# Kernel optimization log

Measured on AMD Instinct MI355X. Metric: run time of the kernel, lower is better.

## Reference

```python
import jax, jax.numpy as jnp
import numpy as np

ALPHA = 0.0005
BETA = 0.1
MARGIN = 100.0
GCN_WEIGHT = 0.1
EPS = 1e-8


def _bce(pred, tgt):
    # torch.nn.BCELoss with mean reduction (pred already in (0,1))
    return -jnp.mean(tgt * jnp.log(pred) + (1.0 - tgt) * jnp.log(1.0 - pred))


def _gcn_loss(nodes, labels, sample_idx):
    # nodes: [B, M, D], labels: [B, M] in {-1,0,1}, sample_idx: [B, S]
    n2 = jnp.sum(nodes * nodes, axis=-1)                               # [B, M]
    s_nodes = jnp.take_along_axis(nodes, sample_idx[:, :, None], axis=1)  # [B, S, D]
    s_lab = jnp.take_along_axis(labels, sample_idx, axis=1)            # [B, S]
    s2 = jnp.take_along_axis(n2, sample_idx, axis=1)                   # [B, S]
    cross = jnp.einsum('bsd,bmd->bsm', s_nodes, nodes)                 # [B, S, M]
    d2 = jnp.maximum(s2[:, :, None] + n2[:, None, :] - 2.0 * cross, 0.0)
    valid = labels >= 0
    same = (labels[:, None, :] == s_lab[:, :, None]) & valid[:, None, :]
    opp = (labels[:, None, :] != s_lab[:, :, None]) & valid[:, None, :]
    BIG = jnp.float32(1e30)
    # farthest same-label node, closest opposite-label node (L2 distance; sqrt is monotone)
    pos_idx = jnp.argmax(jnp.where(same, d2, -BIG), axis=-1)           # [B, S]
    neg_idx = jnp.argmin(jnp.where(opp, d2, BIG), axis=-1)             # [B, S]
    s_norm = jnp.sqrt(s2)

    def _cos(idx):
        dot = jnp.take_along_axis(cross, idx[:, :, None], axis=2)[..., 0]
        nb = jnp.sqrt(jnp.take_along_axis(n2, idx, axis=1))
        return dot / (jnp.maximum(s_norm, EPS) * jnp.maximum(nb, EPS))

    pos_loss = jnp.where(jnp.any(same, axis=-1), _cos(pos_idx), 0.0)
    neg_loss = jnp.where(jnp.any(opp, axis=-1), _cos(neg_idx), 0.0)
    return jnp.sum(pos_loss + neg_loss)


def setup_inputs() -> dict:
    key = jax.random.key(0)
    ks = jax.random.split(key, 10)
    B, T, D, C, M, S = 32, 750, 2048, 20, 750, 64
    score_act = jax.random.uniform(ks[0], (B, C)) * 0.98 + 0.01   # sigmoid-like probs in (0,1)
    score_bkg = jax.random.uniform(ks[1], (B, C)) * 0.98 + 0.01
    feat_act = jax.random.normal(ks[2], (B, T, D))
    feat_bkg = jax.random.normal(ks[3], (B, T, D))
    label = (jax.random.uniform(ks[4], (B, C)) < 0.3).astype(jnp.float32)
    label = label.at[:, 0].set(1.0)  # guarantee >=1 positive class per video
    gt = jax.random.uniform(ks[5], (B, T, C))
    cas = jax.random.normal(ks[6], (B, T, C))
    nodes = jax.random.normal(ks[7], (B, M, D))
    nodes_label = jax.random.randint(ks[8], (B, M), 0, 2)
    sample_idx = jax.random.randint(ks[9], (B, S), 0, M)
    return {'score_act': score_act, 'score_bkg': score_bkg, 'feat_act': feat_act,
            'feat_bkg': feat_bkg, 'label': label, 'gt': gt, 'cas': cas,
            'nodes': nodes, 'nodes_label': nodes_label, 'sample_idx': sample_idx}


def reference(score_act, score_bkg, feat_act, feat_bkg, label, gt, cas, nodes, nodes_label, sample_idx):
    label_n = label / jnp.sum(label, axis=1, keepdims=True)
    loss_cls = _bce(score_act, label_n)
    label_bkg = jnp.ones_like(label) / label.shape[1]
    loss_be = _bce(score_bkg, label_bkg)
    loss_act = jnp.maximum(MARGIN - jnp.linalg.norm(jnp.mean(feat_act, axis=1), axis=1), 0.0)
    loss_bkg = jnp.linalg.norm(jnp.mean(feat_bkg, axis=1), axis=1)
    loss_um = jnp.mean((loss_act + loss_bkg) ** 2)
    loss_gcn = GCN_WEIGHT * _gcn_loss(nodes, nodes_label, sample_idx)
    return loss_cls + ALPHA * loss_um + BETA * loss_be + loss_gcn
```

## Files before the change

kernel.cpp:

```cpp
#include <hip/hip_runtime.h>
#include <math.h>

#define BB 32
#define TT 750
#define DD 2048
#define CC 20
#define MM 750
#define SS 64
#define MT 64
#define NT 12
#define FSPLIT 16
#define FROWS 47
#define FUNITS (2 * BB * FSPLIT)

#define ALPHA_W 0.0005f
#define BETA_W 0.1f
#define MARGIN_W 100.0f
#define GCN_W 0.1f
#define EPS_V 1e-8f

#define WS_LOSS01 0
#define WS_N2ACT 16
#define WS_N2BKG 48
#define WS_GCNB 80
#define WS_S2 128
#define WS_CAND 4096
#define WS_COLSUM 200704

typedef __attribute__((ext_vector_type(8))) short bf16x8;
typedef __attribute__((ext_vector_type(4))) float f32x4;

__device__ __forceinline__ unsigned short f2bf(float f) {
  unsigned int u = __float_as_uint(f);
  return (unsigned short)((u + 0x7FFFu + ((u >> 16) & 1u)) >> 16);
}

__global__ __launch_bounds__(512) void feat_kernel(
    const float* __restrict__ feat_act, const float* __restrict__ feat_bkg,
    float* __restrict__ ws) {
  int u = blockIdx.x;
  int tid = threadIdx.x;
  int tz = u >> 9;
  int rem = u & 511;
  int fb = rem >> 4;
  int sub = rem & 15;
  const float* feat = tz ? feat_bkg : feat_act;
  int t0 = sub * FROWS;
  int t1 = t0 + FROWS < TT ? t0 + FROWS : TT;
  const float* bp = feat + (size_t)fb * TT * DD + tid * 4;

  f32x4 a0 = {0.f, 0.f, 0.f, 0.f}, a1 = {0.f, 0.f, 0.f, 0.f};
  f32x4 a2 = {0.f, 0.f, 0.f, 0.f}, a3 = {0.f, 0.f, 0.f, 0.f};
  int t = t0;
  for (; t + 3 < t1; t += 4) {
    f32x4 v0 = __builtin_nontemporal_load((const f32x4*)(bp + (size_t)t * DD));
    f32x4 v1 =
        __builtin_nontemporal_load((const f32x4*)(bp + (size_t)(t + 1) * DD));
    f32x4 v2 =
        __builtin_nontemporal_load((const f32x4*)(bp + (size_t)(t + 2) * DD));
    f32x4 v3 =
        __builtin_nontemporal_load((const f32x4*)(bp + (size_t)(t + 3) * DD));
    a0 += v0;
    a1 += v1;
    a2 += v2;
    a3 += v3;
  }
  for (; t < t1; ++t)
    a0 += __builtin_nontemporal_load((const f32x4*)(bp + (size_t)t * DD));
  f32x4 r = (a0 + a2) + (a1 + a3);
  float* cs =
      ws + WS_COLSUM + ((size_t)(tz * BB + fb) * FSPLIT + sub) * DD + tid * 4;
  *(f32x4*)cs = r;
}

__global__ __launch_bounds__(256, 3) void gcn_kernel(
    const float* __restrict__ score_act, const float* __restrict__ score_bkg,
    const float* __restrict__ label, const float* __restrict__ nodes,
    const int* __restrict__ nlab, const int* __restrict__ sidx,
    float* __restrict__ ws) {
  int bx = blockIdx.x;
  int tid = threadIdx.x;

  if (bx < NT * BB) {
    int b = bx / NT, tile = bx % NT;

    __shared__ __align__(16) unsigned short sAh[64 * 64];
    __shared__ __align__(16) unsigned short sBh[64 * 64];
    __shared__ float sS2[SS];
    __shared__ float sN2[MT];
    __shared__ int sSlab[SS];
    __shared__ int sMlab[MT];

    if (tid < SS) {
      sSlab[tid] = nlab[b * MM + sidx[b * SS + tid]];
    } else if (tid < SS + MT) {
      int ml = tid - SS;
      int m = tile * MT + ml;
      sMlab[ml] = (m < MM) ? nlab[b * MM + m] : -2;
    }

    int r = tid >> 2, p = tid & 3;
    const float* aRow = nodes + ((size_t)b * MM + sidx[b * SS + r]) * DD;
    int mrow = tile * MT + r;
    bool bval = (mrow < MM);
    const float* bRow = nodes + ((size_t)b * MM + (bval ? mrow : 0)) * DD;

    int wslot[4];
#pragma unroll
    for (int j = 0; j < 4; ++j) {
      int u = p + 4 * j;
      wslot[j] = r * 64 + ((((u >> 1) ^ (r & 7)) << 1) + (u & 1)) * 4;
    }

    int lane = tid & 63, w = tid >> 6;
    int g = lane >> 4, c = lane & 15;

    float aSq = 0.f, bSq = 0.f;
    f32x4 acc[4];
#pragma unroll
    for (int f = 0; f < 4; ++f) acc[f] = (f32x4){0.f, 0.f, 0.f, 0.f};

    float4 pa[4], pb[4];
#pragma unroll
    for (int j = 0; j < 4; ++j) {
      int off = (p + 4 * j) * 4;
      pa[j] = *(const float4*)(aRow + off);
      pb[j] = *(const float4*)(bRow + off);
    }

    for (int ch = 0; ch < 32; ++ch) {
      __syncthreads();
#pragma unroll
      for (int j = 0; j < 4; ++j) {
        float4 v = pa[j];
        aSq += v.x * v.x + v.y * v.y + v.z * v.z + v.w * v.w;
        unsigned int lo = (unsigned int)f2bf(v.x) | ((unsigned int)f2bf(v.y) << 16);
        unsigned int hi = (unsigned int)f2bf(v.z) | ((unsigned int)f2bf(v.w) << 16);
        *(uint2*)&sAh[wslot[j]] = make_uint2(lo, hi);
        float4 t = pb[j];
        bSq += t.x * t.x + t.y * t.y + t.z * t.z + t.w * t.w;
        lo = (unsigned int)f2bf(t.x) | ((unsigned int)f2bf(t.y) << 16);
        hi = (unsigned int)f2bf(t.z) | ((unsigned int)f2bf(t.w) << 16);
        *(uint2*)&sBh[wslot[j]] = make_uint2(lo, hi);
      }
      __syncthreads();
      if (ch < 31) {
        const float* ap = aRow + (ch + 1) * 64;
        const float* bp = bRow + (ch + 1) * 64;
#pragma unroll
        for (int j = 0; j < 4; ++j) {
          int off = (p + 4 * j) * 4;
          pa[j] = *(const float4*)(ap + off);
          pb[j] = *(const float4*)(bp + off);
        }
      }
#pragma unroll
      for (int kk = 0; kk < 2; ++kk) {
        int su = kk * 4 + g;
        int arow = w * 16 + c;
        bf16x8 af = *(const bf16x8*)&sAh[arow * 64 + (su ^ (arow & 7)) * 8];
#pragma unroll
        for (int f = 0; f < 4; ++f) {
          int brow = f * 16 + c;
          bf16x8 bfr = *(const bf16x8*)&sBh[brow * 64 + (su ^ (brow & 7)) * 8];
          acc[f] = __builtin_amdgcn_mfma_f32_16x16x32_bf16(af, bfr, acc[f], 0, 0, 0);
        }
      }
    }

    aSq += __shfl_down(aSq, 2, 4);
    aSq += __shfl_down(aSq, 1, 4);
    bSq += __shfl_down(bSq, 2, 4);
    bSq += __shfl_down(bSq, 1, 4);
    if (p == 0) {
      sS2[r] = aSq;
      sN2[r] = bSq;
    }
    __syncthreads();

    if (tile == 0 && tid < SS) ws[WS_S2 + b * SS + tid] = sS2[tid];

#pragma unroll
    for (int reg = 0; reg < 4; ++reg) {
      int s = w * 16 + g * 4 + reg;
      int slab = sSlab[s];
      float s2v = sS2[s];
      float posD = -3.4e38f, posC = 0.f, posN = 0.f;
      int posI = -1;
      float negD = 3.4e38f, negC = 0.f, negN = 0.f;
      int negI = -1;
#pragma unroll
      for (int f = 0; f < 4; ++f) {
        int ml = f * 16 + c;
        int lab = sMlab[ml];
        float cv = acc[f][reg];
        float n2 = sN2[ml];
        float d2 = fmaxf(s2v + n2 - 2.f * cv, 0.f);
        if (lab >= 0 && lab == slab && (posI < 0 || d2 > posD)) {
          posD = d2; posI = tile * MT + ml; posC = cv; posN = n2;
        }
        if (lab >= 0 && lab != slab && (negI < 0 || d2 < negD)) {
          negD = d2; negI = tile * MT + ml; negC = cv; negN = n2;
        }
      }
#pragma unroll
      for (int off = 8; off; off >>= 1) {
        float oD = __shfl_down(posD, off, 16);
        int oI = __shfl_down(posI, off, 16);
        float oC = __shfl_down(posC, off, 16);
        float oN = __shfl_down(posN, off, 16);
        bool take = (oI >= 0) &&
                    (posI < 0 || oD > posD || (oD == posD && oI < posI));
        if (take) { posD = oD; posI = oI; posC = oC; posN = oN; }
        oD = __shfl_down(negD, off, 16);
        oI = __shfl_down(negI, off, 16);
        oC = __shfl_down(negC, off, 16);
        oN = __shfl_down(negN, off, 16);
        take = (oI >= 0) &&
               (negI < 0 || oD < negD || (oD == negD && oI < negI));
        if (take) { negD = oD; negI = oI; negC = oC; negN = oN; }
      }
      if (c == 0) {
        size_t base = (((size_t)b * SS + s) * NT + tile) * 8;
        *(float4*)&ws[WS_CAND + base] =
            make_float4(posD, __int_as_float(posI), posC, posN);
        *(float4*)&ws[WS_CAND + base + 4] =
            make_float4(negD, __int_as_float(negI), negC, negN);
      }
    }
  } else {
    float vc = 0.f, vb = 0.f;
    for (int i = tid; i < BB * CC; i += 256) {
      int b = i / CC, c = i % CC;
      float rs = 0.f;
      for (int k = 0; k < CC; ++k) rs += label[b * CC + k];
      float ln = label[b * CC + c] / rs;
      float pa = score_act[i];
      vc += ln * logf(pa) + (1.f - ln) * logf(1.f - pa);
      float pb = score_bkg[i];
      const float tb = 1.f / (float)CC;
      vb += tb * logf(pb) + (1.f - tb) * logf(1.f - pb);
    }
    for (int off = 32; off; off >>= 1) {
      vc += __shfl_down(vc, off, 64);
      vb += __shfl_down(vb, off, 64);
    }
    __shared__ float rc[4], rb[4];
    if ((tid & 63) == 0) {
      rc[tid >> 6] = vc;
      rb[tid >> 6] = vb;
    }
    __syncthreads();
    if (tid == 0) {
      ws[WS_LOSS01] = -(rc[0] + rc[1] + rc[2] + rc[3]) / (float)(BB * CC);
      ws[WS_LOSS01 + 1] = -(rb[0] + rb[1] + rb[2] + rb[3]) / (float)(BB * CC);
    }
  }
}

__global__ __launch_bounds__(256) void tail_kernel(float* __restrict__ ws) {
  int bx = blockIdx.x, tid = threadIdx.x;
  if (bx < 64) {
    int tz = bx >> 5, fb = bx & 31;
    const float* cs = ws + WS_COLSUM + (size_t)(tz * BB + fb) * FSPLIT * DD;
    int d0 = tid * 8;
    float4 A0 = make_float4(0.f, 0.f, 0.f, 0.f);
    float4 A1 = make_float4(0.f, 0.f, 0.f, 0.f);
    for (int blk = 0; blk < FSPLIT; ++blk) {
      const float* pp = cs + blk * DD + d0;
      float4 u = *(const float4*)pp;
      float4 v = *(const float4*)(pp + 4);
      A0.x += u.x; A0.y += u.y; A0.z += u.z; A0.w += u.w;
      A1.x += v.x; A1.y += v.y; A1.z += v.z; A1.w += v.w;
    }
    const float inv = 1.f / (float)TT;
    float m0 = A0.x * inv, m1 = A0.y * inv, m2 = A0.z * inv, m3 = A0.w * inv;
    float m4 = A1.x * inv, m5 = A1.y * inv, m6 = A1.z * inv, m7 = A1.w * inv;
    float v = m0 * m0 + m1 * m1 + m2 * m2 + m3 * m3 +
              m4 * m4 + m5 * m5 + m6 * m6 + m7 * m7;
    for (int off = 32; off; off >>= 1) v += __shfl_down(v, off, 64);
    __shared__ float red[4];
    if ((tid & 63) == 0) red[tid >> 6] = v;
    __syncthreads();
    if (tid == 0)
      ws[(tz ? WS_N2BKG : WS_N2ACT) + fb] = red[0] + red[1] + red[2] + red[3];
  } else {
    int b = bx - 64;
    if (tid < SS) {
      const float* cb = ws + WS_CAND + ((size_t)b * SS + tid) * NT * 8;
      float posD = -3.4e38f, posC = 0.f, posN = 0.f;
      int posI = -1;
      float negD = 3.4e38f, negC = 0.f, negN = 0.f;
      int negI = -1;
      for (int t = 0; t < NT; ++t) {
        float4 pq = *(const float4*)&cb[t * 8];
        int oI = __float_as_int(pq.y);
        if (oI >= 0 && (posI < 0 || pq.x > posD || (pq.x == posD && oI < posI))) {
          posD = pq.x; posI = oI; posC = pq.z; posN = pq.w;
        }
        float4 qq = *(const float4*)&cb[t * 8 + 4];
        oI = __float_as_int(qq.y);
        if (oI >= 0 && (negI < 0 || qq.x < negD || (qq.x == negD && oI < negI))) {
          negD = qq.x; negI = oI; negC = qq.z; negN = qq.w;
        }
      }
      float snorm = sqrtf(ws[WS_S2 + b * SS + tid]);
      float sden = fmaxf(snorm, EPS_V);
      float pl = (posI >= 0) ? posC / (sden * fmaxf(sqrtf(posN), EPS_V)) : 0.f;
      float nl = (negI >= 0) ? negC / (sden * fmaxf(sqrtf(negN), EPS_V)) : 0.f;
      float v = pl + nl;
      for (int off = 32; off; off >>= 1) v += __shfl_down(v, off, 64);
      if (tid == 0) ws[WS_GCNB + b] = v;
    }
  }
}

__global__ void final_kernel(const float* __restrict__ ws,
                             float* __restrict__ out) {
  int tid = threadIdx.x;
  float um = 0.f, g = 0.f;
  if (tid < BB) {
    float la = fmaxf(MARGIN_W - sqrtf(ws[WS_N2ACT + tid]), 0.f);
    float lb = sqrtf(ws[WS_N2BKG + tid]);
    um = (la + lb) * (la + lb);
    g = ws[WS_GCNB + tid];
  }
  for (int off = 32; off; off >>= 1) {
    um += __shfl_down(um, off, 64);
    g += __shfl_down(g, off, 64);
  }
  if (tid == 0)
    out[0] = ws[WS_LOSS01] + BETA_W * ws[WS_LOSS01 + 1] +
             ALPHA_W * (um / (float)BB) + GCN_W * g;
}

extern "C" void kernel_launch(void* const* d_in, const int* in_sizes, int n_in,
                              void* d_out, int out_size, void* d_ws,
                              size_t ws_size, hipStream_t stream) {
  const float* score_act = (const float*)d_in[0];
  const float* score_bkg = (const float*)d_in[1];
  const float* feat_act = (const float*)d_in[2];
  const float* feat_bkg = (const float*)d_in[3];
  const float* label = (const float*)d_in[4];
  const float* nodes = (const float*)d_in[7];
  const int* nlab = (const int*)d_in[8];
  const int* sidx = (const int*)d_in[9];
  float* out = (float*)d_out;
  float* wsf = (float*)d_ws;

  feat_kernel<<<FUNITS, 512, 0, stream>>>(feat_act, feat_bkg, wsf);
  gcn_kernel<<<NT * BB + 1, 256, 0, stream>>>(score_act, score_bkg, label,
                                              nodes, nlab, sidx, wsf);
  tail_kernel<<<96, 256, 0, stream>>>(wsf);
  final_kernel<<<1, 64, 0, stream>>>(wsf, out);
}
```

Baseline: 127.0 us.

## Fuse feature-sum and GCN kernels into one interleaved mega kernel

Merges the memory-bound feature column-sum kernel and the MFMA-based GCN distance kernel into one 512-thread launch. Block indices are interleaved, 3 GCN blocks per 16 feature blocks, so compute-heavy and bandwidth-heavy work run concurrently on the GPU. Each GCN block now handles two node tiles that share one staged sample tile, which halves the redundant loads of the sampled rows. The risk is that the shared launch bounds and LDS footprint lower occupancy for the streaming feature blocks.

Result: no change. 128.6 us (+1.2%).

```diff
diff --git a/kernel.cpp b/kernel.cpp
--- a/kernel.cpp
+++ b/kernel.cpp
@@ -9,9 +9,13 @@
 #define SS 64
 #define MT 64
 #define NT 12
+#define NPAIR 6
 #define FSPLIT 16
 #define FROWS 47
 #define FUNITS (2 * BB * FSPLIT)
+
+#define GCNP_BLOCKS (NPAIR * BB)
+#define TOT_BLOCKS (GCNP_BLOCKS + FUNITS + 1)
 
 #define ALPHA_W 0.0005f
 #define BETA_W 0.1f
@@ -35,154 +39,142 @@
   return (unsigned short)((u + 0x7FFFu + ((u >> 16) & 1u)) >> 16);
 }
 
-__global__ __launch_bounds__(512) void feat_kernel(
+__global__ __launch_bounds__(512, 4) void mega_kernel(
+    const float* __restrict__ score_act, const float* __restrict__ score_bkg,
     const float* __restrict__ feat_act, const float* __restrict__ feat_bkg,
-    float* __restrict__ ws) {
-  int u = blockIdx.x;
-  int tid = threadIdx.x;
-  int tz = u >> 9;
-  int rem = u & 511;
-  int fb = rem >> 4;
-  int sub = rem & 15;
-  const float* feat = tz ? feat_bkg : feat_act;
-  int t0 = sub * FROWS;
-  int t1 = t0 + FROWS < TT ? t0 + FROWS : TT;
-  const float* bp = feat + (size_t)fb * TT * DD + tid * 4;
-
-  f32x4 a0 = {0.f, 0.f, 0.f, 0.f}, a1 = {0.f, 0.f, 0.f, 0.f};
-  f32x4 a2 = {0.f, 0.f, 0.f, 0.f}, a3 = {0.f, 0.f, 0.f, 0.f};
-  int t = t0;
-  for (; t + 3 < t1; t += 4) {
-    f32x4 v0 = __builtin_nontemporal_load((const f32x4*)(bp + (size_t)t * DD));
-    f32x4 v1 =
-        __builtin_nontemporal_load((const f32x4*)(bp + (size_t)(t + 1) * DD));
-    f32x4 v2 =
-        __builtin_nontemporal_load((const f32x4*)(bp + (size_t)(t + 2) * DD));
-    f32x4 v3 =
-        __builtin_nontemporal_load((const f32x4*)(bp + (size_t)(t + 3) * DD));
-    a0 += v0;
-    a1 += v1;
-    a2 += v2;
-    a3 += v3;
-  }
-  for (; t < t1; ++t)
-    a0 += __builtin_nontemporal_load((const f32x4*)(bp + (size_t)t * DD));
-  f32x4 r = (a0 + a2) + (a1 + a3);
-  float* cs =
-      ws + WS_COLSUM + ((size_t)(tz * BB + fb) * FSPLIT + sub) * DD + tid * 4;
-  *(f32x4*)cs = r;
-}
-
-__global__ __launch_bounds__(256, 3) void gcn_kernel(
-    const float* __restrict__ score_act, const float* __restrict__ score_bkg,
     const float* __restrict__ label, const float* __restrict__ nodes,
     const int* __restrict__ nlab, const int* __restrict__ sidx,
     float* __restrict__ ws) {
   int bx = blockIdx.x;
   int tid = threadIdx.x;
-
-  if (bx < NT * BB) {
-    int b = bx / NT, tile = bx % NT;
+  int q19 = bx / 19, r19 = bx % 19;
+
+  if (bx < TOT_BLOCKS - 1 && r19 < 3) {
+    int idx = q19 * 3 + r19;
+    int b = idx / NPAIR, pair = idx % NPAIR;
+    int tileBase = pair * 2;
 
     __shared__ __align__(16) unsigned short sAh[64 * 64];
-    __shared__ __align__(16) unsigned short sBh[64 * 64];
+    __shared__ __align__(16) unsigned short sBh[2][64 * 64];
     __shared__ float sS2[SS];
-    __shared__ float sN2[MT];
+    __shared__ float sN2[2][MT];
     __shared__ int sSlab[SS];
-    __shared__ int sMlab[MT];
+    __shared__ int sMlab[2][MT];
 
     if (tid < SS) {
       sSlab[tid] = nlab[b * MM + sidx[b * SS + tid]];
-    } else if (tid < SS + MT) {
-      int ml = tid - SS;
-      int m = tile * MT + ml;
-      sMlab[ml] = (m < MM) ? nlab[b * MM + m] : -2;
-    }
-
-    int r = tid >> 2, p = tid & 3;
+    } else if (tid < SS + 2 * MT) {
+      int q = tid - SS;
+      int grp = q >> 6, ml = q & 63;
+      int m = (tileBase + grp) * MT + ml;
+      sMlab[grp][ml] = (m < MM) ? nlab[b * MM + m] : -2;
+    }
+
+    int r = tid >> 3, p = tid & 7;
     const float* aRow = nodes + ((size_t)b * MM + sidx[b * SS + r]) * DD;
-    int mrow = tile * MT + r;
-    bool bval = (mrow < MM);
-    const float* bRow = nodes + ((size_t)b * MM + (bval ? mrow : 0)) * DD;
-
-    int wslot[4];
-#pragma unroll
-    for (int j = 0; j < 4; ++j) {
-      int u = p + 4 * j;
+    int m0row = tileBase * MT + r;
+    const float* b0Row = nodes + ((size_t)b * MM + m0row) * DD;
+    int m1row = (tileBase + 1) * MT + r;
+    bool b1val = (m1row < MM);
+    const float* b1Row = nodes + ((size_t)b * MM + (b1val ? m1row : 0)) * DD;
+
+    int wslot[2];
+#pragma unroll
+    for (int j = 0; j < 2; ++j) {
+      int u = p + 8 * j;
       wslot[j] = r * 64 + ((((u >> 1) ^ (r & 7)) << 1) + (u & 1)) * 4;
     }
 
     int lane = tid & 63, w = tid >> 6;
+    int grp = w >> 2, w4 = w & 3;
     int g = lane >> 4, c = lane & 15;
 
-    float aSq = 0.f, bSq = 0.f;
+    float aSq = 0.f, b0Sq = 0.f, b1Sq = 0.f;
     f32x4 acc[4];
 #pragma unroll
     for (int f = 0; f < 4; ++f) acc[f] = (f32x4){0.f, 0.f, 0.f, 0.f};
 
-    float4 pa[4], pb[4];
-#pragma unroll
-    for (int j = 0; j < 4; ++j) {
-      int off = (p + 4 * j) * 4;
+    float4 pa[2], pb0[2], pb1[2];
+#pragma unroll
+    for (int j = 0; j < 2; ++j) {
+      int off = (p + 8 * j) * 4;
       pa[j] = *(const float4*)(aRow + off);
-      pb[j] = *(const float4*)(bRow + off);
+      pb0[j] = *(const float4*)(b0Row + off);
+      pb1[j] = b1val ? *(const float4*)(b1Row + off)
+                     : make_float4(0.f, 0.f, 0.f, 0.f);
     }
 
     for (int ch = 0; ch < 32; ++ch) {
       __syncthreads();
 #pragma unroll
-      for (int j = 0; j < 4; ++j) {
+      for (int j = 0; j < 2; ++j) {
         float4 v = pa[j];
         aSq += v.x * v.x + v.y * v.y + v.z * v.z + v.w * v.w;
         unsigned int lo = (unsigned int)f2bf(v.x) | ((unsigned int)f2bf(v.y) << 16);
         unsigned int hi = (unsigned int)f2bf(v.z) | ((unsigned int)f2bf(v.w) << 16);
         *(uint2*)&sAh[wslot[j]] = make_uint2(lo, hi);
-        float4 t = pb[j];
-        bSq += t.x * t.x + t.y * t.y + t.z * t.z + t.w * t.w;
-        lo = (unsigned int)f2bf(t.x) | ((unsigned int)f2bf(t.y) << 16);
-        hi = (unsigned int)f2bf(t.z) | ((unsigned int)f2bf(t.w) << 16);
-        *(uint2*)&sBh[wslot[j]] = make_uint2(lo, hi);
+        float4 t0 = pb0[j];
+        b0Sq += t0.x * t0.x + t0.y * t0.y + t0.z * t0.z + t0.w * t0.w;
+        lo = (unsigned int)f2bf(t0.x) | ((unsigned int)f2bf(t0.y) << 16);
+        hi = (unsigned int)f2bf(t0.z) | ((unsigned int)f2bf(t0.w) << 16);
+        *(uint2*)&sBh[0][wslot[j]] = make_uint2(lo, hi);
+        float4 t1 = pb1[j];
+        b1Sq += t1.x * t1.x + t1.y * t1.y + t1.z * t1.z + t1.w * t1.w;
+        lo = (unsigned int)f2bf(t1.x) | ((unsigned int)f2bf(t1.y) << 16);
+        hi = (unsigned int)f2bf(t1.z) | ((unsigned int)f2bf(t1.w) << 16);
+        *(uint2*)&sBh[1][wslot[j]] = make_uint2(lo, hi);
       }
       __syncthreads();
       if (ch < 31) {
         const float* ap = aRow + (ch + 1) * 64;
-        const float* bp = bRow + (ch + 1) * 64;
-#pragma unroll
-        for (int j = 0; j < 4; ++j) {
-          int off = (p + 4 * j) * 4;
+        const float* b0p = b0Row + (ch + 1) * 64;
+        const float* b1p = b1Row + (ch + 1) * 64;
+#pragma unroll
+        for (int j = 0; j < 2; ++j) {
+          int off = (p + 8 * j) * 4;
           pa[j] = *(const float4*)(ap + off);
-          pb[j] = *(const float4*)(bp + off);
+          pb0[j] = *(const float4*)(b0p + off);
+          pb1[j] = b1val ? *(const float4*)(b1p + off)
+                         : make_float4(0.f, 0.f, 0.f, 0.f);
         }
       }
 #pragma unroll
       for (int kk = 0; kk < 2; ++kk) {
         int su = kk * 4 + g;
-        int arow = w * 16 + c;
+        int arow = w4 * 16 + c;
         bf16x8 af = *(const bf16x8*)&sAh[arow * 64 + (su ^ (arow & 7)) * 8];
 #pragma unroll
         for (int f = 0; f < 4; ++f) {
           int brow = f * 16 + c;
-          bf16x8 bfr = *(const bf16x8*)&sBh[brow * 64 + (su ^ (brow & 7)) * 8];
+          bf16x8 bfr =
+              *(const bf16x8*)&sBh[grp][brow * 64 + (su ^ (brow & 7)) * 8];
           acc[f] = __builtin_amdgcn_mfma_f32_16x16x32_bf16(af, bfr, acc[f], 0, 0, 0);
         }
       }
     }
 
-    aSq += __shfl_down(aSq, 2, 4);
-    aSq += __shfl_down(aSq, 1, 4);
-    bSq += __shfl_down(bSq, 2, 4);
-    bSq += __shfl_down(bSq, 1, 4);
+    aSq += __shfl_down(aSq, 4, 8);
+    aSq += __shfl_down(aSq, 2, 8);
+    aSq += __shfl_down(aSq, 1, 8);
+    b0Sq += __shfl_down(b0Sq, 4, 8);
+    b0Sq += __shfl_down(b0Sq, 2, 8);
+    b0Sq += __shfl_down(b0Sq, 1, 8);
+    b1Sq += __shfl_down(b1Sq, 4, 8);
+    b1Sq += __shfl_down(b1Sq, 2, 8);
+    b1Sq += __shfl_down(b1Sq, 1, 8);
     if (p == 0) {
       sS2[r] = aSq;
-      sN2[r] = bSq;
+      sN2[0][r] = b0Sq;
+      sN2[1][r] = b1Sq;
     }
     __syncthreads();
 
-    if (tile == 0 && tid < SS) ws[WS_S2 + b * SS + tid] = sS2[tid];
-
+    if (pair == 0 && tid < SS) ws[WS_S2 + b * SS + tid] = sS2[tid];
+
+    int tile = tileBase + grp;
 #pragma unroll
     for (int reg = 0; reg < 4; ++reg) {
-      int s = w * 16 + g * 4 + reg;
+      int s = w4 * 16 + g * 4 + reg;
       int slab = sSlab[s];
       float s2v = sS2[s];
       float posD = -3.4e38f, posC = 0.f, posN = 0.f;
@@ -192,9 +184,9 @@
 #pragma unroll
       for (int f = 0; f < 4; ++f) {
         int ml = f * 16 + c;
-        int lab = sMlab[ml];
+        int lab = sMlab[grp][ml];
         float cv = acc[f][reg];
-        float n2 = sN2[ml];
+        float n2 = sN2[grp][ml];
         float d2 = fmaxf(s2v + n2 - 2.f * cv, 0.f);
         if (lab >= 0 && lab == slab && (posI < 0 || d2 > posD)) {
           posD = d2; posI = tile * MT + ml; posC = cv; posN = n2;
@@ -228,9 +220,42 @@
             make_float4(negD, __int_as_float(negI), negC, negN);
       }
     }
+  } else if (bx < TOT_BLOCKS - 1) {
+    int u = q19 * 16 + (r19 - 3);
+    int tz = u >> 9;
+    int rem = u & 511;
+    int fb = rem >> 4;
+    int sub = rem & 15;
+    const float* feat = tz ? feat_bkg : feat_act;
+    int t0 = sub * FROWS;
+    int t1 = t0 + FROWS < TT ? t0 + FROWS : TT;
+    const float* bp = feat + (size_t)fb * TT * DD + tid * 4;
+
+    f32x4 a0 = {0.f, 0.f, 0.f, 0.f}, a1 = {0.f, 0.f, 0.f, 0.f};
+    f32x4 a2 = {0.f, 0.f, 0.f, 0.f}, a3 = {0.f, 0.f, 0.f, 0.f};
+    int t = t0;
+    for (; t + 3 < t1; t += 4) {
+      f32x4 v0 = __builtin_nontemporal_load((const f32x4*)(bp + (size_t)t * DD));
+      f32x4 v1 =
+          __builtin_nontemporal_load((const f32x4*)(bp + (size_t)(t + 1) * DD));
+      f32x4 v2 =
+          __builtin_nontemporal_load((const f32x4*)(bp + (size_t)(t + 2) * DD));
+      f32x4 v3 =
+          __builtin_nontemporal_load((const f32x4*)(bp + (size_t)(t + 3) * DD));
+      a0 += v0;
+      a1 += v1;
+      a2 += v2;
+      a3 += v3;
+    }
+    for (; t < t1; ++t)
+      a0 += __builtin_nontemporal_load((const f32x4*)(bp + (size_t)t * DD));
+    f32x4 rr = (a0 + a2) + (a1 + a3);
+    float* cs = ws + WS_COLSUM +
+                ((size_t)(tz * BB + fb) * FSPLIT + sub) * DD + tid * 4;
+    *(f32x4*)cs = rr;
   } else {
     float vc = 0.f, vb = 0.f;
-    for (int i = tid; i < BB * CC; i += 256) {
+    for (int i = tid; i < BB * CC; i += 512) {
       int b = i / CC, c = i % CC;
       float rs = 0.f;
       for (int k = 0; k < CC; ++k) rs += label[b * CC + k];
@@ -245,15 +270,20 @@
       vc += __shfl_down(vc, off, 64);
       vb += __shfl_down(vb, off, 64);
     }
-    __shared__ float rc[4], rb[4];
+    __shared__ float rc[8], rb[8];
     if ((tid & 63) == 0) {
       rc[tid >> 6] = vc;
       rb[tid >> 6] = vb;
     }
     __syncthreads();
     if (tid == 0) {
-      ws[WS_LOSS01] = -(rc[0] + rc[1] + rc[2] + rc[3]) / (float)(BB * CC);
-      ws[WS_LOSS01 + 1] = -(rb[0] + rb[1] + rb[2] + rb[3]) / (float)(BB * CC);
+      float sc = 0.f, sb = 0.f;
+      for (int k = 0; k < 8; ++k) {
+        sc += rc[k];
+        sb += rb[k];
+      }
+      ws[WS_LOSS01] = -sc / (float)(BB * CC);
+      ws[WS_LOSS01 + 1] = -sb / (float)(BB * CC);
     }
   }
 }
@@ -348,9 +378,8 @@
   float* out = (float*)d_out;
   float* wsf = (float*)d_ws;
 
-  feat_kernel<<<FUNITS, 512, 0, stream>>>(feat_act, feat_bkg, wsf);
-  gcn_kernel<<<NT * BB + 1, 256, 0, stream>>>(score_act, score_bkg, label,
-                                              nodes, nlab, sidx, wsf);
+  mega_kernel<<<TOT_BLOCKS, 512, 0, stream>>>(
+      score_act, score_bkg, feat_act, feat_bkg, label, nodes, nlab, sidx, wsf);
   tail_kernel<<<96, 256, 0, stream>>>(wsf);
   final_kernel<<<1, 64, 0, stream>>>(wsf, out);
 }
```
